# Performance work log

Hardware: AMD Instinct MI355X
Metric: run time of the kernel (lower is better)

Reference implementation:

```python
import jax, jax.numpy as jnp
import numpy as np

N = 40000; E = 512000; F = 128; H = 4; C = 32; HC = 128; G = 64; FC = 48


def _bn(x, g, b):
    # BatchNorm1d in training mode: batch stats, biased variance, eps=1e-5
    mu = jnp.mean(x, 0)
    var = jnp.var(x, 0)
    return g * (x - mu) * jax.lax.rsqrt(var + 1e-5) + b


def _gat(x, src, dst, W, a_s, a_d, bias):
    # PyG GATConv: linear -> per-head edge scores -> self-loops -> LeakyReLU ->
    # segment softmax over incoming edges of each target -> weighted scatter-add
    n = x.shape[0]
    h = (x @ W).reshape(n, H, C)
    es = jnp.einsum('nhc,hc->nh', h, a_s)  # source-side score
    ed = jnp.einsum('nhc,hc->nh', h, a_d)  # target-side score
    loop = jnp.arange(n, dtype=src.dtype)
    s = jnp.concatenate([src, loop])
    d = jnp.concatenate([dst, loop])
    e = jax.nn.leaky_relu(es[s] + ed[d], 0.2)  # [E+N, H]
    m = jax.ops.segment_max(e, d, num_segments=n)
    ex = jnp.exp(e - m[d])
    den = jax.ops.segment_sum(ex, d, num_segments=n)
    alpha = ex / den[d]
    out = jax.ops.segment_sum(h[s] * alpha[:, :, None], d, num_segments=n)
    return out.reshape(n, H * C) + bias


def _pool(x, batch, aw, ab):
    # graph_attention_pool: per-graph softmax over node scores, weighted scatter-add
    sc = x @ aw + ab  # [N,1]
    m = jax.ops.segment_max(sc, batch, num_segments=G)
    ex = jnp.exp(sc - m[batch])
    den = jax.ops.segment_sum(ex, batch, num_segments=G)
    a = ex / den[batch]
    return jax.ops.segment_sum(x * a, batch, num_segments=G)  # [G, HC]


def _forward(x1, x2, W0, as0, ad0, b0, W1, as1, ad1, b1, W2, as2, ad2, b2,
             g1, be1, g2, be2, g3, be3, att_w, att_b, fci_w, fci_b, gbi, bbi,
             fcw, fcb, fc1w, fc1b, gf1, bf1, fc2w, fc2b,
             edge_index1, batch1, edge_index2, batch2):
    def branch(x, ei):
        src, dst = ei[0], ei[1]
        x = jax.nn.relu(_bn(_gat(x, src, dst, W0, as0, ad0, b0), g1, be1))
        x = jax.nn.relu(_bn(_gat(x, src, dst, W1, as1, ad1, b1), g2, be2))
        x = jax.nn.relu(_bn(_gat(x, src, dst, W2, as2, ad2, b2), g3, be3))
        return x
    h1 = branch(x1, edge_index1)
    h2 = branch(x2, edge_index2)
    def head(h, batch):
        p = _pool(h, batch, att_w, att_b)
        z = jax.nn.relu(_bn(p @ fci_w + fci_b, gbi, bbi))
        return z @ fcw + fcb  # note: bn_fc is never applied in the source forward
    o = jnp.concatenate([head(h1, batch1), head(h2, batch2)], axis=-1)
    o = jax.nn.relu(_bn(o @ fc1w + fc1b, gf1, bf1))
    o = o @ fc2w + fc2b
    return jax.nn.sigmoid(o).squeeze(-1)  # [G]


def setup_inputs() -> dict:
    key = jax.random.key(0)
    ks = jax.random.split(key, 24)
    def rn(i, shape, scale=1.0):
        return jax.random.normal(ks[i], shape, jnp.float32) * scale
    inp = {}
    inp['x1'] = rn(0, (N, F))
    inp['x2'] = rn(1, (N, F))
    inp['edge_index1'] = jax.random.randint(ks[2], (2, E), 0, N, dtype=jnp.int32)
    inp['edge_index2'] = jax.random.randint(ks[3], (2, E), 0, N, dtype=jnp.int32)
    inp['batch1'] = jnp.sort(jax.random.randint(ks[4], (N,), 0, G, dtype=jnp.int32))
    inp['batch2'] = jnp.sort(jax.random.randint(ks[5], (N,), 0, G, dtype=jnp.int32))
    inp['W0'] = rn(6, (F, HC), F ** -0.5)
    inp['as0'] = rn(7, (H, C), C ** -0.5)
    inp['ad0'] = rn(8, (H, C), C ** -0.5)
    inp['b0'] = jnp.zeros((HC,), jnp.float32)
    inp['W1'] = rn(9, (HC, HC), HC ** -0.5)
    inp['as1'] = rn(10, (H, C), C ** -0.5)
    inp['ad1'] = rn(11, (H, C), C ** -0.5)
    inp['b1'] = jnp.zeros((HC,), jnp.float32)
    inp['W2'] = rn(12, (HC, HC), HC ** -0.5)
    inp['as2'] = rn(13, (H, C), C ** -0.5)
    inp['ad2'] = rn(14, (H, C), C ** -0.5)
    inp['b2'] = jnp.zeros((HC,), jnp.float32)
    for nm, dim in (('g1', HC), ('g2', HC), ('g3', HC), ('gbi', FC), ('gf1', FC // 4)):
        inp[nm] = jnp.ones((dim,), jnp.float32)
    for nm, dim in (('be1', HC), ('be2', HC), ('be3', HC), ('bbi', FC), ('bf1', FC // 4)):
        inp[nm] = jnp.zeros((dim,), jnp.float32)
    inp['att_w'] = rn(15, (HC, 1), HC ** -0.5)
    inp['att_b'] = jnp.zeros((1,), jnp.float32)
    inp['fci_w'] = rn(16, (HC, FC), HC ** -0.5)
    inp['fci_b'] = jnp.zeros((FC,), jnp.float32)
    inp['fcw'] = rn(17, (FC, FC // 4), FC ** -0.5)
    inp['fcb'] = jnp.zeros((FC // 4,), jnp.float32)
    inp['fc1w'] = rn(18, (FC // 4 * 2, FC // 4), (FC // 2) ** -0.5)
    inp['fc1b'] = jnp.zeros((FC // 4,), jnp.float32)
    inp['fc2w'] = rn(19, (FC // 4, 1), (FC // 4) ** -0.5)
    inp['fc2b'] = jnp.zeros((1,), jnp.float32)
    return inp


def reference(x1, x2, edge_index1, edge_index2, batch1, batch2,
              W0, as0, ad0, b0, W1, as1, ad1, b1, W2, as2, ad2, b2,
              g1, g2, g3, gbi, gf1, be1, be2, be3, bbi, bf1,
              att_w, att_b, fci_w, fci_b, fcw, fcb, fc1w, fc1b, fc2w, fc2b):
    return _forward(x1, x2, W0, as0, ad0, b0, W1, as1, ad1, b1, W2, as2, ad2, b2,
                    g1, be1, g2, be2, g3, be3, att_w, att_b, fci_w, fci_b, gbi, bbi,
                    fcw, fcb, fc1w, fc1b, gf1, bf1, fc2w, fc2b,
                    edge_index1, batch1, edge_index2, batch2)
```

## Files before the change

### kernel.cpp

```cpp
#include <hip/hip_runtime.h>

#define NN 40000
#define EE 512000
#define NB 157
#define BCAP 8000

typedef unsigned short u16;
typedef __attribute__((ext_vector_type(8))) short bf16x8;
typedef __attribute__((ext_vector_type(4))) float f32x4;

__device__ __forceinline__ float bf2f(u16 u) { return __uint_as_float(((unsigned)u) << 16); }
__device__ __forceinline__ u16 f2bf(float f) {
    unsigned u = __float_as_uint(f);
    u += 0x7FFFu + ((u >> 16) & 1u);
    return (u16)(u >> 16);
}
__device__ __forceinline__ unsigned pack2(float a, float b) {
    return (unsigned)f2bf(a) | ((unsigned)f2bf(b) << 16);
}
__device__ __forceinline__ float lrelu(float t) { return t > 0.f ? t : 0.2f * t; }

__global__ __launch_bounds__(256) void detect_k(const u16* __restrict__ x, int* __restrict__ flag) {
    int t = threadIdx.x;
    int cnt = 0;
    for (int j = 0; j < 8; ++j) {
        float v = bf2f(x[(t * 8 + j) * 2]);
        float a = fabsf(v);
        if (a >= 0.00390625f && a <= 256.0f) cnt++;
    }
    __shared__ int sh[256];
    sh[t] = cnt;
    __syncthreads();
    for (int off = 128; off > 0; off >>= 1) {
        if (t < off) sh[t] += sh[t + off];
        __syncthreads();
    }
    if (t == 0) flag[0] = (sh[0] > 1024) ? 1 : 0;
}

struct CvtArgs {
    const void* src[28];
    float* dst[28];
    int n[28];
};

__global__ __launch_bounds__(256) void cvt_k(CvtArgs a, const int* __restrict__ flag) {
    int b = blockIdx.x;
    int n = a.n[b];
    float* d = a.dst[b];
    if (*flag) {
        const u16* p = (const u16*)a.src[b];
        for (int i = threadIdx.x; i < n; i += 256) d[i] = bf2f(p[i]);
    } else {
        const float* p = (const float*)a.src[b];
        for (int i = threadIdx.x; i < n; i += 256) d[i] = p[i];
    }
}

__global__ __launch_bounds__(256) void wtb_k(const float* __restrict__ wcvt, u16* __restrict__ Wtb) {
    int l = blockIdx.x;
    const float* W = wcvt + l * 16640;
    u16* D = Wtb + l * 16384;
    for (int i = threadIdx.x; i < 16384; i += 256) {
        int n = i >> 7, k = i & 127;
        D[i] = f2bf(W[k * 128 + n]);
    }
}

__global__ __launch_bounds__(256) void bucket_k(const int* __restrict__ ei1,
                                                const int* __restrict__ ei2,
                                                int* __restrict__ gcnt,
                                                int2* __restrict__ buf) {
    __shared__ int lh[NB];
    __shared__ int lbase[NB];
    __shared__ int loff[NB];
    int branch = blockIdx.x >= 500;
    int blk = blockIdx.x - (branch ? 500 : 0);
    const int* ei = branch ? ei2 : ei1;
    int gb0 = branch * NB;
    int tid = threadIdx.x;
    for (int i = tid; i < NB; i += 256) lh[i] = 0;
    __syncthreads();
    int e0 = blk * 1024 + tid;
    int sv[4], dv[4], bv[4];
#pragma unroll
    for (int j = 0; j < 4; ++j) {
        int e = e0 + j * 256;
        int d = ei[EE + e];
        int s = ei[e];
        if ((unsigned)d >= NN) d = -1;
        if ((unsigned)s >= NN) s = 0;
        dv[j] = d;
        sv[j] = s;
        bv[j] = d >> 8;
        if (d >= 0 && (unsigned)bv[j] < NB) atomicAdd(&lh[bv[j]], 1);
        else dv[j] = -1;
    }
    __syncthreads();
    for (int i = tid; i < NB; i += 256) {
        int c = lh[i];
        lbase[i] = c ? atomicAdd(&gcnt[gb0 + i], c) : 0;
        loff[i] = 0;
    }
    __syncthreads();
#pragma unroll
    for (int j = 0; j < 4; ++j) {
        if (dv[j] >= 0) {
            int b = bv[j];
            int p = lbase[b] + atomicAdd(&loff[b], 1);
            if ((unsigned)p < BCAP) buf[(size_t)(gb0 + b) * BCAP + p] = (int2){sv[j], dv[j]};
        }
    }
}

__global__ __launch_bounds__(256) void build_k(const int* __restrict__ gcnt,
                                               const int2* __restrict__ buf,
                                               int* __restrict__ fill,
                                               int* __restrict__ csrc) {
    __shared__ int lf[256];
    int branch = blockIdx.x >= NB;
    int b = blockIdx.x - (branch ? NB : 0);
    int tid = threadIdx.x;
    lf[tid] = 0;
    __syncthreads();
    int n = gcnt[branch * NB + b];
    if (n < 0) n = 0;
    if (n > BCAP) n = BCAP;
    int d0 = b << 8;
    size_t soff = (size_t)branch * NN;
    const int2* bp = buf + (size_t)(branch * NB + b) * BCAP;
    for (int i = tid; i < n; i += 256) {
        int2 p = bp[i];
        unsigned loc = (unsigned)(p.y - d0);
        if (loc < 256u && (unsigned)p.y < NN && (unsigned)p.x < NN) {
            int pos = atomicAdd(&lf[loc], 1);
            if ((unsigned)pos < 64u) csrc[(soff + p.y) * 64 + pos] = p.x;
        }
    }
    __syncthreads();
    int d = d0 + tid;
    if (d < NN) fill[soff + d] = lf[tid];
}

__global__ __launch_bounds__(256) void matmul_mfma_k(const void* __restrict__ X1,
                                                     const void* __restrict__ X2,
                                                     const u16* __restrict__ Abase,
                                                     int mode,
                                                     const int* __restrict__ flag,
                                                     const float* __restrict__ bnc,
                                                     const u16* __restrict__ Wtb,
                                                     const float* __restrict__ asf,
                                                     const float* __restrict__ adf,
                                                     u16* __restrict__ Hbase,
                                                     float* __restrict__ es, float* __restrict__ ed) {
    __shared__ u16 Xs[64 * 136];
    __shared__ float scs[128], shs[128];
    int tid = threadIdx.x;
    int branch = blockIdx.x >= 625;
    int blk = blockIdx.x - (branch ? 625 : 0);
    size_t boff = (size_t)branch * NN;
    size_t row0 = (size_t)blk * 64;
    if (mode == 1) {
        if (tid < 128) {
            scs[tid] = bnc[branch * 256 + tid];
            shs[tid] = bnc[branch * 256 + 128 + tid];
        }
        __syncthreads();
        const uint2* X2p = reinterpret_cast<const uint2*>(Abase + (boff + row0) * 128);
        for (int i = tid; i < 2048; i += 256) {
            uint2 p = X2p[i];
            int r = i >> 5, c0 = (i & 31) * 4;
            float v0 = fmaf(bf2f((u16)(p.x & 0xffffu)), scs[c0], shs[c0]);
            float v1 = fmaf(bf2f((u16)(p.x >> 16)), scs[c0 + 1], shs[c0 + 1]);
            float v2 = fmaf(bf2f((u16)(p.y & 0xffffu)), scs[c0 + 2], shs[c0 + 2]);
            float v3 = fmaf(bf2f((u16)(p.y >> 16)), scs[c0 + 3], shs[c0 + 3]);
            v0 = v0 > 0.f ? v0 : 0.f; v1 = v1 > 0.f ? v1 : 0.f;
            v2 = v2 > 0.f ? v2 : 0.f; v3 = v3 > 0.f ? v3 : 0.f;
            unsigned* dst = (unsigned*)(Xs + r * 136 + c0);
            dst[0] = pack2(v0, v1);
            dst[1] = pack2(v2, v3);
        }
    } else {
        const void* Xv = branch ? X2 : X1;
        if (*flag) {
            const uint2* X2p = reinterpret_cast<const uint2*>((const u16*)Xv + row0 * 128);
            for (int i = tid; i < 2048; i += 256) {
                uint2 p = X2p[i];
                int r = i >> 5, c0 = (i & 31) * 4;
                unsigned* dst = (unsigned*)(Xs + r * 136 + c0);
                dst[0] = p.x;
                dst[1] = p.y;
            }
        } else {
            const float4* X4 = reinterpret_cast<const float4*>((const float*)Xv + row0 * 128);
            for (int i = tid; i < 2048; i += 256) {
                float4 v = X4[i];
                int r = i >> 5, c0 = (i & 31) * 4;
                unsigned* dst = (unsigned*)(Xs + r * 136 + c0);
                dst[0] = pack2(v.x, v.y);
                dst[1] = pack2(v.z, v.w);
            }
        }
    }
    __syncthreads();
    int w = tid >> 6, l = tid & 63;
    int q = l >> 4, c = l & 15;
    int mrow = w * 16;
    f32x4 acc[8];
#pragma unroll
    for (int t = 0; t < 8; ++t) acc[t] = (f32x4){0.f, 0.f, 0.f, 0.f};
#pragma unroll
    for (int ks = 0; ks < 4; ++ks) {
        int k0 = ks * 32;
        bf16x8 afrag = *(const bf16x8*)(Xs + (mrow + c) * 136 + k0 + q * 8);
#pragma unroll
        for (int t = 0; t < 8; ++t) {
            bf16x8 bfrag = *(const bf16x8*)(Wtb + (t * 16 + c) * 128 + k0 + q * 8);
            acc[t] = __builtin_amdgcn_mfma_f32_16x16x32_bf16(afrag, bfrag, acc[t], 0, 0, 0);
        }
    }
    float esp[4][4] = {}, edp[4][4] = {};
#pragma unroll
    for (int t = 0; t < 8; ++t) {
        float av = asf[t * 16 + c], dv = adf[t * 16 + c];
        int h = t >> 1;
#pragma unroll
        for (int r = 0; r < 4; ++r) {
            esp[h][r] = fmaf(acc[t][r], av, esp[h][r]);
            edp[h][r] = fmaf(acc[t][r], dv, edp[h][r]);
        }
    }
#pragma unroll
    for (int h = 0; h < 4; ++h)
#pragma unroll
        for (int r = 0; r < 4; ++r) {
            esp[h][r] += __shfl_xor(esp[h][r], 1, 64);
            esp[h][r] += __shfl_xor(esp[h][r], 2, 64);
            esp[h][r] += __shfl_xor(esp[h][r], 4, 64);
            esp[h][r] += __shfl_xor(esp[h][r], 8, 64);
            edp[h][r] += __shfl_xor(edp[h][r], 1, 64);
            edp[h][r] += __shfl_xor(edp[h][r], 2, 64);
            edp[h][r] += __shfl_xor(edp[h][r], 4, 64);
            edp[h][r] += __shfl_xor(edp[h][r], 8, 64);
        }
    if (c < 4) {
#pragma unroll
        for (int r = 0; r < 4; ++r) {
            size_t grow = boff + row0 + mrow + q * 4 + r;
            es[grow * 4 + c] = esp[c][r];
            ed[grow * 4 + c] = edp[c][r];
        }
    }
    __syncthreads();
    u16* Cs = Xs;
#pragma unroll
    for (int t = 0; t < 8; ++t)
#pragma unroll
        for (int r = 0; r < 4; ++r)
            Cs[(mrow + q * 4 + r) * 128 + t * 16 + c] = f2bf(acc[t][r]);
    __syncthreads();
    uint2* yp = (uint2*)(Hbase + (boff + row0) * 128);
    const uint2* cs2 = (const uint2*)Cs;
    for (int i = tid; i < 2048; i += 256) yp[i] = cs2[i];
}

__global__ __launch_bounds__(256) void agg_k(const u16* __restrict__ hb, const float* __restrict__ es,
                                             const float* __restrict__ ed, const int* __restrict__ fill,
                                             const int* __restrict__ csrc, u16* __restrict__ Ab,
                                             float* __restrict__ bktbase, int l) {
    __shared__ float ss[512], qq[512];
    int gwid = (blockIdx.x * 256 + threadIdx.x) >> 6;
    int branch = gwid >= NN;
    size_t srow = branch ? (size_t)NN : 0;
    int lane = threadIdx.x & 63;
    int deg = fill[gwid];
    if (deg > 64) deg = 64;
    if (deg < 0) deg = 0;
    size_t rs = (size_t)gwid * 64;
    int head = lane >> 4;
    int h4 = lane & 3;
    float edn = ed[gwid * 4 + head];
    float edn4 = ed[gwid * 4 + h4];
    float acc0, acc1, den;
    {
        float w = __expf(lrelu(es[gwid * 4 + head] + edn));
        den = w;
        unsigned pv = ((const unsigned*)(hb + (size_t)gwid * 128))[lane];
        acc0 = w * bf2f((u16)(pv & 0xffffu));
        acc1 = w * bf2f((u16)(pv >> 16));
    }
    int myj = lane >> 2;
    for (int i = 0; i < deg; i += 8) {
        float myw = 0.f;
        if (lane < 32) {
            int idx = i + myj;
            if (idx < deg) {
                int s_ = csrc[rs + idx];
                myw = __expf(lrelu(es[(srow + s_) * 4 + h4] + edn4));
            }
        }
        unsigned pv[8];
        int nv = deg - i;
#pragma unroll
        for (int j = 0; j < 8; ++j) {
            if (j < nv) {
                int s_ = csrc[rs + i + j];
                pv[j] = ((const unsigned*)(hb + (srow + s_) * 128))[lane];
            } else {
                pv[j] = 0u;
            }
        }
#pragma unroll
        for (int j = 0; j < 8; ++j) {
            float wj = __shfl(myw, (j << 2) | head, 64);
            den += wj;
            acc0 = fmaf(wj, bf2f((u16)(pv[j] & 0xffffu)), acc0);
            acc1 = fmaf(wj, bf2f((u16)(pv[j] >> 16)), acc1);
        }
    }
    float inv = 1.0f / den;
    float v0 = acc0 * inv, v1 = acc1 * inv;
    ((unsigned*)Ab)[(size_t)gwid * 64 + lane] = (unsigned)f2bf(v0) | ((unsigned)f2bf(v1) << 16);
    int w = threadIdx.x >> 6;
    ss[w * 128 + 2 * lane] = v0;      ss[w * 128 + 2 * lane + 1] = v1;
    qq[w * 128 + 2 * lane] = v0 * v0; qq[w * 128 + 2 * lane + 1] = v1 * v1;
    __syncthreads();
    int t = threadIdx.x;
    float* dst = bktbase + (branch * 3 + l) * 16384 + (blockIdx.x & 63) * 256;
    if (t < 128) {
        atomicAdd(&dst[t], ss[t] + ss[128 + t] + ss[256 + t] + ss[384 + t]);
    } else {
        int f = t - 128;
        atomicAdd(&dst[t], qq[f] + qq[128 + f] + qq[256 + f] + qq[384 + f]);
    }
}

__global__ __launch_bounds__(256) void bnconst_k(const float* __restrict__ bktbase, int l,
                                                 const float* __restrict__ gam,
                                                 const float* __restrict__ bet,
                                                 float* __restrict__ bnc) {
    __shared__ float red[256];
    int b = blockIdx.x;
    const float* bkt = bktbase + (b * 3 + l) * 16384;
    int tid = threadIdx.x;
    float s = 0.f;
    for (int k = 0; k < 64; ++k) s += bkt[k * 256 + tid];
    red[tid] = s;
    __syncthreads();
    if (tid < 128) {
        float mu = red[tid] * (1.0f / NN);
        float var = red[128 + tid] * (1.0f / NN) - mu * mu;
        float sc_ = rsqrtf(var + 1e-5f) * gam[tid];
        bnc[b * 256 + tid] = sc_;
        bnc[b * 256 + 128 + tid] = bet[tid] - mu * sc_;
    }
}

__global__ __launch_bounds__(256) void pool_score_k(const u16* __restrict__ Ab,
                                                    const float* __restrict__ bnc,
                                                    const float* __restrict__ attw,
                                                    float* __restrict__ scw) {
    int tid = threadIdx.x;
    int gwid = (blockIdx.x * 256 + tid) >> 6;
    int branch = gwid >= NN;
    const float* bncp = bnc + branch * 256;
    int lane = tid & 63;
    int f0 = 2 * lane, f1 = 2 * lane + 1;
    unsigned pv = ((const unsigned*)Ab)[(size_t)gwid * 64 + lane];
    float v0 = fmaf(bf2f((u16)(pv & 0xffffu)), bncp[f0], bncp[128 + f0]); v0 = v0 > 0.f ? v0 : 0.f;
    float v1 = fmaf(bf2f((u16)(pv >> 16)), bncp[f1], bncp[128 + f1]);     v1 = v1 > 0.f ? v1 : 0.f;
    float v = v0 * attw[f0] + v1 * attw[f1];
    for (int off = 1; off < 64; off <<= 1) v += __shfl_xor(v, off, 64);
    if (lane == 0) scw[gwid] = __expf(v);
}

__device__ __forceinline__ int lower_bound_dev(const int* __restrict__ b, int n, int v) {
    int lo = 0, hi = n;
    while (lo < hi) {
        int mid = (lo + hi) >> 1;
        if (b[mid] < v) lo = mid + 1; else hi = mid;
    }
    return lo;
}

__global__ __launch_bounds__(256) void pool_den_k(const float* __restrict__ scw,
                                                  const int* __restrict__ batch1,
                                                  const int* __restrict__ batch2,
                                                  float* __restrict__ gden) {
    int branch = blockIdx.x >= 64;
    int g = blockIdx.x - (branch ? 64 : 0);
    const int* batch = branch ? batch2 : batch1;
    const float* sc = scw + (size_t)branch * NN;
    int tid = threadIdx.x;
    int start = lower_bound_dev(batch, NN, g);
    int end = lower_bound_dev(batch, NN, g + 1);
    __shared__ float sh[256];
    float s = 0.f;
    for (int i = start + tid; i < end; i += 256) s += sc[i];
    sh[tid] = s;
    __syncthreads();
    for (int off = 128; off > 0; off >>= 1) {
        if (tid < off) sh[tid] += sh[tid + off];
        __syncthreads();
    }
    if (tid == 0) gden[blockIdx.x] = (sh[0] > 1e-30f) ? sh[0] : 1e-30f;
}

__global__ __launch_bounds__(256) void pool_accum2_k(const u16* __restrict__ Ab,
                                                     const float* __restrict__ scw,
                                                     const int* __restrict__ batch1,
                                                     const int* __restrict__ batch2,
                                                     const float* __restrict__ gden,
                                                     const float* __restrict__ bnc,
                                                     float* __restrict__ pooled) {
    __shared__ float wsh[64];
    __shared__ int gsh[64];
    int branch = blockIdx.x >= 625;
    int blk = blockIdx.x - (branch ? 625 : 0);
    const int* batch = branch ? batch2 : batch1;
    size_t boff = (size_t)branch * NN;
    int r0 = blk * 64;
    int tid = threadIdx.x;
    if (tid < 64) {
        int g = batch[r0 + tid];
        if ((unsigned)g >= 64) g = 0;
        gsh[tid] = g;
        wsh[tid] = scw[boff + r0 + tid] / gden[branch * 64 + g];
    }
    __syncthreads();
    const float* bncp = bnc + branch * 256;
    float* poolp = pooled + (size_t)branch * 8192;
    int f = tid & 127, half = tid >> 7;
    float bs = bncp[f], bb = bncp[128 + f];
    float racc = 0.f;
    int curg = gsh[half];
    for (int r = half; r < 64; r += 2) {
        int g = gsh[r];
        if (g != curg) {
            atomicAdd(&poolp[curg * 128 + f], racc);
            racc = 0.f;
            curg = g;
        }
        float v = fmaf(bf2f(Ab[(boff + r0 + r) * 128 + f]), bs, bb);
        v = v > 0.f ? v : 0.f;
        racc = fmaf(wsh[r], v, racc);
    }
    atomicAdd(&poolp[curg * 128 + f], racc);
}

__global__ __launch_bounds__(256) void headA_k(const float* __restrict__ pooled,
                                               const float* __restrict__ fciw, const float* __restrict__ fcib,
                                               float* __restrict__ Tall) {
    __shared__ float Wl[6144];
    __shared__ float Pl[128];
    int tid = threadIdx.x;
    int g = blockIdx.x;
    for (int i = tid; i < 6144; i += 256) Wl[i] = fciw[i];
    if (tid < 128) Pl[tid] = pooled[g * 128 + tid];
    __syncthreads();
    if (tid < 48) {
        float s = fcib[tid];
        for (int k = 0; k < 128; ++k) s = fmaf(Pl[k], Wl[k * 48 + tid], s);
        Tall[g * 48 + tid] = s;
    }
}

__global__ __launch_bounds__(256) void headB_k(const float* __restrict__ Tall,
                                               const float* __restrict__ gbi, const float* __restrict__ bbi,
                                               const float* __restrict__ fcw, const float* __restrict__ fcb,
                                               const float* __restrict__ fc1w, const float* __restrict__ fc1b,
                                               const float* __restrict__ gf1, const float* __restrict__ bf1,
                                               const float* __restrict__ fc2w, const float* __restrict__ fc2b,
                                               void* __restrict__ out, const int* __restrict__ flag) {
    __shared__ float T[6144];
    __shared__ float X[64 * 24];
    __shared__ float Y[64 * 12];
    __shared__ float st[192];
    __shared__ float st2[24];
    __shared__ float wl[576 + 288 + 12 + 12 + 12 + 12 + 48 + 48 + 1];
    float* fcw_l  = wl;
    float* fc1w_l = wl + 576;
    float* fcb_l  = wl + 864;
    float* fc1b_l = wl + 876;
    float* gf1_l  = wl + 888;
    float* bf1_l  = wl + 900;
    float* gbi_l  = wl + 912;
    float* bbi_l  = wl + 960;
    float* fc2b_l = wl + 1008;
    __shared__ float fc2w_l[12];
    int tid = threadIdx.x;
    for (int i = tid; i < 6144; i += 256) T[i] = Tall[i];
    for (int i = tid; i < 576; i += 256) fcw_l[i] = fcw[i];
    for (int i = tid; i < 288; i += 256) fc1w_l[i] = fc1w[i];
    if (tid < 12) {
        fcb_l[tid] = fcb[tid]; fc1b_l[tid] = fc1b[tid];
        gf1_l[tid] = gf1[tid]; bf1_l[tid] = bf1[tid];
        fc2w_l[tid] = fc2w[tid];
    }
    if (tid < 48) { gbi_l[tid] = gbi[tid]; bbi_l[tid] = bbi[tid]; }
    if (tid == 0) fc2b_l[0] = fc2b[0];
    __syncthreads();
    if (tid < 96) {
        int b = tid / 48, c = tid - b * 48;
        float s = 0.f, ss = 0.f;
        for (int g = 0; g < 64; ++g) { float v = T[b * 3072 + g * 48 + c]; s += v; ss += v * v; }
        float mu = s * (1.f / 64), var = ss * (1.f / 64) - mu * mu;
        float sc_ = rsqrtf(var + 1e-5f) * gbi_l[c];
        st[tid] = sc_;
        st[96 + tid] = bbi_l[c] - mu * sc_;
    }
    __syncthreads();
    for (int i = tid; i < 6144; i += 256) {
        int b = i / 3072, c = i % 48;
        int col = b * 48 + c;
        float v = fmaf(T[i], st[col], st[96 + col]);
        T[i] = v > 0.f ? v : 0.f;
    }
    __syncthreads();
    for (int idx = tid; idx < 1536; idx += 256) {
        int b = idx / 768, r = idx - b * 768;
        int g = r / 12, c = r - g * 12;
        float s = fcb_l[c];
        const float* tr = T + b * 3072 + g * 48;
        for (int k = 0; k < 48; ++k) s = fmaf(tr[k], fcw_l[k * 12 + c], s);
        X[g * 24 + b * 12 + c] = s;
    }
    __syncthreads();
    for (int idx = tid; idx < 768; idx += 256) {
        int g = idx / 12, c = idx - g * 12;
        float s = fc1b_l[c];
        const float* xr = X + g * 24;
        for (int k = 0; k < 24; ++k) s = fmaf(xr[k], fc1w_l[k * 12 + c], s);
        Y[idx] = s;
    }
    __syncthreads();
    if (tid < 12) {
        float s = 0.f, ss = 0.f;
        for (int g = 0; g < 64; ++g) { float v = Y[g * 12 + tid]; s += v; ss += v * v; }
        float mu = s * (1.f / 64), var = ss * (1.f / 64) - mu * mu;
        float sc_ = rsqrtf(var + 1e-5f) * gf1_l[tid];
        st2[tid] = sc_;
        st2[12 + tid] = bf1_l[tid] - mu * sc_;
    }
    __syncthreads();
    if (tid < 64) {
        float s = fc2b_l[0];
        for (int k = 0; k < 12; ++k) {
            float v = fmaf(Y[tid * 12 + k], st2[k], st2[12 + k]);
            v = v > 0.f ? v : 0.f;
            s = fmaf(v, fc2w_l[k], s);
        }
        float sig = 1.f / (1.f + __expf(-s));
        if (*flag) ((u16*)out)[tid] = f2bf(sig);
        else       ((float*)out)[tid] = sig;
    }
}

extern "C" void kernel_launch(void* const* d_in, const int* in_sizes, int n_in,
                              void* d_out, int out_size, void* d_ws, size_t ws_size,
                              hipStream_t stream) {
    const void* xin[2]  = {d_in[0], d_in[1]};
    const int* ei[2]    = {(const int*)d_in[2], (const int*)d_in[3]};
    const int* batch[2] = {(const int*)d_in[4], (const int*)d_in[5]};

    char* ws = (char*)d_ws;
    u16*   Hb     = (u16*)(ws + 0);
    u16*   Ab     = (u16*)(ws + 20480000);
    float* es     = (float*)(ws + 40960000);
    float* ed     = (float*)(ws + 42240000);
    float* scw    = (float*)(ws + 43520000);
    int*   fill   = (int*)(ws + 43840000);
    int*   csrc   = (int*)(ws + 44160000);
    float* wcvt   = (float*)(ws + 64640000);
    u16*   Wtb    = (u16*)(ws + 64880000);
    float* zbase  = (float*)(ws + 64978304);
    float* bkt    = zbase;
    float* pooled = zbase + 98304;
    int*   gcnt   = (int*)(zbase + 114688);
    float* gden   = zbase + 115008;
    float* bnc    = zbase + 115136;
    float* Tall   = zbase + 115648;
    int*   flag   = (int*)(zbase + 121792);

    static const int widx[28] = {6,7,8, 10,11,12, 14,15,16, 18,19,20, 23,24,25,
                                 21,26, 22,27, 28, 30,31, 32,33, 34,35, 36,37};
    static const int wn[28]   = {16384,128,128, 16384,128,128, 16384,128,128, 128,128,128,
                                 128,128,128, 48,48, 12,12, 128, 6144,48, 576,12, 288,12, 12,1};
    CvtArgs ca;
    float* wptr[28];
    {
        size_t off = 0;
        for (int i = 0; i < 28; ++i) {
            ca.src[i] = d_in[widx[i]];
            ca.dst[i] = wcvt + off;
            ca.n[i] = wn[i];
            wptr[i] = wcvt + off;
            off += wn[i];
        }
    }
    const float* asf[3] = {wptr[1], wptr[4], wptr[7]};
    const float* adf[3] = {wptr[2], wptr[5], wptr[8]};
    const float* gf[3]  = {wptr[9], wptr[10], wptr[11]};
    const float* bef[3] = {wptr[12], wptr[13], wptr[14]};
    const float *gbi = wptr[15], *bbi = wptr[16], *gf1 = wptr[17], *bf1 = wptr[18];
    const float *attw = wptr[19], *fciw = wptr[20], *fcib = wptr[21];
    const float *fcw = wptr[22], *fcb = wptr[23], *fc1w = wptr[24], *fc1b = wptr[25];
    const float *fc2w = wptr[26], *fc2b = wptr[27];

    detect_k<<<1, 256, 0, stream>>>((const u16*)d_in[0], flag);
    cvt_k<<<28, 256, 0, stream>>>(ca, flag);
    wtb_k<<<3, 256, 0, stream>>>(wcvt, Wtb);
    (void)hipMemsetAsync(zbase, 0, (98304 + 16384 + 320) * sizeof(float), stream);

    bucket_k<<<1000, 256, 0, stream>>>(ei[0], ei[1], gcnt, (int2*)Hb);
    build_k<<<2 * NB, 256, 0, stream>>>(gcnt, (const int2*)Hb, fill, csrc);

    for (int l = 0; l < 3; ++l) {
        matmul_mfma_k<<<1250, 256, 0, stream>>>(xin[0], xin[1], Ab, l == 0 ? 0 : 1, flag,
                                                bnc, Wtb + l * 16384, asf[l], adf[l],
                                                Hb, es, ed);
        agg_k<<<20000, 256, 0, stream>>>(Hb, es, ed, fill, csrc, Ab, bkt, l);
        bnconst_k<<<2, 256, 0, stream>>>(bkt, l, gf[l], bef[l], bnc);
    }
    pool_score_k<<<20000, 256, 0, stream>>>(Ab, bnc, attw, scw);
    pool_den_k<<<128, 256, 0, stream>>>(scw, batch[0], batch[1], gden);
    pool_accum2_k<<<1250, 256, 0, stream>>>(Ab, scw, batch[0], batch[1], gden, bnc, pooled);
    headA_k<<<128, 256, 0, stream>>>(pooled, fciw, fcib, Tall);
    headB_k<<<1, 256, 0, stream>>>(Tall, gbi, bbi, fcw, fcb, fc1w, fc1b, gf1, bf1,
                                   fc2w, fc2b, d_out, flag);
}
```

Measured before the change: 690.6 us.

## Fuse graph pooling stages into one per-graph kernel and simplify edge weight compute

Replaces the four pooling/head-A kernels (score, denominator, atomic accumulate, first FC) with one kernel that runs one block per graph. Each block computes the attention scores into shared memory, reduces the denominator, accumulates the pooled vector and applies the first FC layer. This removes intermediate global buffers, atomics and launches, but uses only 128 blocks and silently caps graphs at 2048 nodes. In agg_k, every lane now computes its own edge weight rather than having 32 lanes compute and broadcast via shuffle, trading redundant exp work for fewer cross-lane dependencies.

```diff
diff --git a/kernel.cpp b/kernel.cpp
--- a/kernel.cpp
+++ b/kernel.cpp
@@ -278,9 +278,7 @@
     if (deg < 0) deg = 0;
     size_t rs = (size_t)gwid * 64;
     int head = lane >> 4;
-    int h4 = lane & 3;
     float edn = ed[gwid * 4 + head];
-    float edn4 = ed[gwid * 4 + h4];
     float acc0, acc1, den;
     {
         float w = __expf(lrelu(es[gwid * 4 + head] + edn));
@@ -289,33 +287,26 @@
         acc0 = w * bf2f((u16)(pv & 0xffffu));
         acc1 = w * bf2f((u16)(pv >> 16));
     }
-    int myj = lane >> 2;
     for (int i = 0; i < deg; i += 8) {
-        float myw = 0.f;
-        if (lane < 32) {
-            int idx = i + myj;
-            if (idx < deg) {
-                int s_ = csrc[rs + idx];
-                myw = __expf(lrelu(es[(srow + s_) * 4 + h4] + edn4));
-            }
-        }
+        int nv = deg - i;
+        float wv[8];
         unsigned pv[8];
-        int nv = deg - i;
 #pragma unroll
         for (int j = 0; j < 8; ++j) {
             if (j < nv) {
                 int s_ = csrc[rs + i + j];
+                wv[j] = __expf(lrelu(es[(srow + s_) * 4 + head] + edn));
                 pv[j] = ((const unsigned*)(hb + (srow + s_) * 128))[lane];
             } else {
+                wv[j] = 0.f;
                 pv[j] = 0u;
             }
         }
 #pragma unroll
         for (int j = 0; j < 8; ++j) {
-            float wj = __shfl(myw, (j << 2) | head, 64);
-            den += wj;
-            acc0 = fmaf(wj, bf2f((u16)(pv[j] & 0xffffu)), acc0);
-            acc1 = fmaf(wj, bf2f((u16)(pv[j] >> 16)), acc1);
+            den += wv[j];
+            acc0 = fmaf(wv[j], bf2f((u16)(pv[j] & 0xffffu)), acc0);
+            acc1 = fmaf(wv[j], bf2f((u16)(pv[j] >> 16)), acc1);
         }
     }
     float inv = 1.0f / den;
@@ -356,24 +347,6 @@
     }
 }
 
-__global__ __launch_bounds__(256) void pool_score_k(const u16* __restrict__ Ab,
-                                                    const float* __restrict__ bnc,
-                                                    const float* __restrict__ attw,
-                                                    float* __restrict__ scw) {
-    int tid = threadIdx.x;
-    int gwid = (blockIdx.x * 256 + tid) >> 6;
-    int branch = gwid >= NN;
-    const float* bncp = bnc + branch * 256;
-    int lane = tid & 63;
-    int f0 = 2 * lane, f1 = 2 * lane + 1;
-    unsigned pv = ((const unsigned*)Ab)[(size_t)gwid * 64 + lane];
-    float v0 = fmaf(bf2f((u16)(pv & 0xffffu)), bncp[f0], bncp[128 + f0]); v0 = v0 > 0.f ? v0 : 0.f;
-    float v1 = fmaf(bf2f((u16)(pv >> 16)), bncp[f1], bncp[128 + f1]);     v1 = v1 > 0.f ? v1 : 0.f;
-    float v = v0 * attw[f0] + v1 * attw[f1];
-    for (int off = 1; off < 64; off <<= 1) v += __shfl_xor(v, off, 64);
-    if (lane == 0) scw[gwid] = __expf(v);
-}
-
 __device__ __forceinline__ int lower_bound_dev(const int* __restrict__ b, int n, int v) {
     int lo = 0, hi = n;
     while (lo < hi) {
@@ -383,85 +356,73 @@
     return lo;
 }
 
-__global__ __launch_bounds__(256) void pool_den_k(const float* __restrict__ scw,
-                                                  const int* __restrict__ batch1,
-                                                  const int* __restrict__ batch2,
-                                                  float* __restrict__ gden) {
+__global__ __launch_bounds__(256) void pool_fused_k(const u16* __restrict__ Ab,
+                                                    const float* __restrict__ bnc,
+                                                    const float* __restrict__ attw,
+                                                    const int* __restrict__ batch1,
+                                                    const int* __restrict__ batch2,
+                                                    const float* __restrict__ fciw,
+                                                    const float* __restrict__ fcib,
+                                                    float* __restrict__ Tall) {
+    __shared__ float wsh[2048];
+    __shared__ float red[256];
+    __shared__ float ssum[512];
+    __shared__ float Pl[128];
+    __shared__ float Wl[6144];
     int branch = blockIdx.x >= 64;
     int g = blockIdx.x - (branch ? 64 : 0);
     const int* batch = branch ? batch2 : batch1;
-    const float* sc = scw + (size_t)branch * NN;
+    size_t boff = (size_t)branch * NN;
     int tid = threadIdx.x;
+    int w = tid >> 6, lane = tid & 63;
+    for (int i = tid; i < 6144; i += 256) Wl[i] = fciw[i];
     int start = lower_bound_dev(batch, NN, g);
     int end = lower_bound_dev(batch, NN, g + 1);
-    __shared__ float sh[256];
+    int cnt = end - start;
+    if (cnt < 0) cnt = 0;
+    if (cnt > 2048) cnt = 2048;
+    const float* bncp = bnc + branch * 256;
+    int f0 = 2 * lane, f1 = f0 + 1;
+    float bs0 = bncp[f0], bb0 = bncp[128 + f0];
+    float bs1 = bncp[f1], bb1 = bncp[128 + f1];
+    float aw0 = attw[f0], aw1 = attw[f1];
+    for (int i = w; i < cnt; i += 4) {
+        unsigned pv = ((const unsigned*)Ab)[(boff + start + i) * 64 + lane];
+        float v0 = fmaf(bf2f((u16)(pv & 0xffffu)), bs0, bb0); v0 = v0 > 0.f ? v0 : 0.f;
+        float v1 = fmaf(bf2f((u16)(pv >> 16)), bs1, bb1);     v1 = v1 > 0.f ? v1 : 0.f;
+        float v = v0 * aw0 + v1 * aw1;
+        for (int off = 1; off < 64; off <<= 1) v += __shfl_xor(v, off, 64);
+        if (lane == 0) wsh[i] = __expf(v);
+    }
+    __syncthreads();
     float s = 0.f;
-    for (int i = start + tid; i < end; i += 256) s += sc[i];
-    sh[tid] = s;
+    for (int i = tid; i < cnt; i += 256) s += wsh[i];
+    red[tid] = s;
     __syncthreads();
     for (int off = 128; off > 0; off >>= 1) {
-        if (tid < off) sh[tid] += sh[tid + off];
+        if (tid < off) red[tid] += red[tid + off];
         __syncthreads();
     }
-    if (tid == 0) gden[blockIdx.x] = (sh[0] > 1e-30f) ? sh[0] : 1e-30f;
-}
-
-__global__ __launch_bounds__(256) void pool_accum2_k(const u16* __restrict__ Ab,
-                                                     const float* __restrict__ scw,
-                                                     const int* __restrict__ batch1,
-                                                     const int* __restrict__ batch2,
-                                                     const float* __restrict__ gden,
-                                                     const float* __restrict__ bnc,
-                                                     float* __restrict__ pooled) {
-    __shared__ float wsh[64];
-    __shared__ int gsh[64];
-    int branch = blockIdx.x >= 625;
-    int blk = blockIdx.x - (branch ? 625 : 0);
-    const int* batch = branch ? batch2 : batch1;
-    size_t boff = (size_t)branch * NN;
-    int r0 = blk * 64;
-    int tid = threadIdx.x;
-    if (tid < 64) {
-        int g = batch[r0 + tid];
-        if ((unsigned)g >= 64) g = 0;
-        gsh[tid] = g;
-        wsh[tid] = scw[boff + r0 + tid] / gden[branch * 64 + g];
-    }
-    __syncthreads();
-    const float* bncp = bnc + branch * 256;
-    float* poolp = pooled + (size_t)branch * 8192;
-    int f = tid & 127, half = tid >> 7;
-    float bs = bncp[f], bb = bncp[128 + f];
-    float racc = 0.f;
-    int curg = gsh[half];
-    for (int r = half; r < 64; r += 2) {
-        int g = gsh[r];
-        if (g != curg) {
-            atomicAdd(&poolp[curg * 128 + f], racc);
-            racc = 0.f;
-            curg = g;
-        }
-        float v = fmaf(bf2f(Ab[(boff + r0 + r) * 128 + f]), bs, bb);
-        v = v > 0.f ? v : 0.f;
-        racc = fmaf(wsh[r], v, racc);
-    }
-    atomicAdd(&poolp[curg * 128 + f], racc);
-}
-
-__global__ __launch_bounds__(256) void headA_k(const float* __restrict__ pooled,
-                                               const float* __restrict__ fciw, const float* __restrict__ fcib,
-                                               float* __restrict__ Tall) {
-    __shared__ float Wl[6144];
-    __shared__ float Pl[128];
-    int tid = threadIdx.x;
-    int g = blockIdx.x;
-    for (int i = tid; i < 6144; i += 256) Wl[i] = fciw[i];
-    if (tid < 128) Pl[tid] = pooled[g * 128 + tid];
+    float den = red[0];
+    float inv = 1.0f / ((den > 1e-30f) ? den : 1e-30f);
+    float r0 = 0.f, r1 = 0.f;
+    for (int i = w; i < cnt; i += 4) {
+        unsigned pv = ((const unsigned*)Ab)[(boff + start + i) * 64 + lane];
+        float v0 = fmaf(bf2f((u16)(pv & 0xffffu)), bs0, bb0); v0 = v0 > 0.f ? v0 : 0.f;
+        float v1 = fmaf(bf2f((u16)(pv >> 16)), bs1, bb1);     v1 = v1 > 0.f ? v1 : 0.f;
+        float wt = wsh[i] * inv;
+        r0 = fmaf(wt, v0, r0);
+        r1 = fmaf(wt, v1, r1);
+    }
+    ssum[w * 128 + f0] = r0;
+    ssum[w * 128 + f1] = r1;
+    __syncthreads();
+    if (tid < 128) Pl[tid] = ssum[tid] + ssum[128 + tid] + ssum[256 + tid] + ssum[384 + tid];
     __syncthreads();
     if (tid < 48) {
-        float s = fcib[tid];
-        for (int k = 0; k < 128; ++k) s = fmaf(Pl[k], Wl[k * 48 + tid], s);
-        Tall[g * 48 + tid] = s;
+        float acc = fcib[tid];
+        for (int k = 0; k < 128; ++k) acc = fmaf(Pl[k], Wl[k * 48 + tid], acc);
+        Tall[blockIdx.x * 48 + tid] = acc;
     }
 }
 
@@ -568,16 +529,13 @@
     u16*   Ab     = (u16*)(ws + 20480000);
     float* es     = (float*)(ws + 40960000);
     float* ed     = (float*)(ws + 42240000);
-    float* scw    = (float*)(ws + 43520000);
     int*   fill   = (int*)(ws + 43840000);
     int*   csrc   = (int*)(ws + 44160000);
     float* wcvt   = (float*)(ws + 64640000);
     u16*   Wtb    = (u16*)(ws + 64880000);
     float* zbase  = (float*)(ws + 64978304);
     float* bkt    = zbase;
-    float* pooled = zbase + 98304;
     int*   gcnt   = (int*)(zbase + 114688);
-    float* gden   = zbase + 115008;
     float* bnc    = zbase + 115136;
     float* Tall   = zbase + 115648;
     int*   flag   = (int*)(zbase + 121792);
@@ -622,10 +580,8 @@
         agg_k<<<20000, 256, 0, stream>>>(Hb, es, ed, fill, csrc, Ab, bkt, l);
         bnconst_k<<<2, 256, 0, stream>>>(bkt, l, gf[l], bef[l], bnc);
     }
-    pool_score_k<<<20000, 256, 0, stream>>>(Ab, bnc, attw, scw);
-    pool_den_k<<<128, 256, 0, stream>>>(scw, batch[0], batch[1], gden);
-    pool_accum2_k<<<1250, 256, 0, stream>>>(Ab, scw, batch[0], batch[1], gden, bnc, pooled);
-    headA_k<<<128, 256, 0, stream>>>(pooled, fciw, fcib, Tall);
+    pool_fused_k<<<128, 256, 0, stream>>>(Ab, bnc, attw, batch[0], batch[1],
+                                          fciw, fcib, Tall);
     headB_k<<<1, 256, 0, stream>>>(Tall, gbi, bbi, fcw, fcb, fc1w, fc1b, gf1, bf1,
                                    fc2w, fc2b, d_out, flag);
 }
```

Result: slower. 816.2 us (+18.2%).
